# Optimization experiments

Hardware: AMD Instinct MI355X
Metric: run time of the kernel (lower is better)

Reference implementation:

```python
import jax, jax.numpy as jnp
import numpy as np

N, E, F_IN, HID, L_EXTRA, G = 50000, 800000, 128, 128, 3, 256

def gcn_conv(x, W, b, src, dst, norm):
    # PyG GCNConv: out = D^-1/2 (A+I) D^-1/2 (X W) + b  (self-loops included in src/dst)
    xw = x @ W                                  # [N, out]
    msg = xw[src] * norm[:, None]               # [E+N, out]
    return jax.ops.segment_sum(msg, dst, num_segments=N) + b

def setup_inputs() -> dict:
    key = jax.random.key(0)
    ks = jax.random.split(key, 12)
    x = jax.random.normal(ks[0], (N, F_IN), dtype=jnp.float32)
    edge_index = jax.random.randint(ks[1], (2, E), 0, N, dtype=jnp.int64)
    batch = jnp.sort(jax.random.randint(ks[2], (N,), 0, G, dtype=jnp.int64))
    s = 1.0 / np.sqrt(HID)
    W0 = jax.random.uniform(ks[3], (F_IN, HID), jnp.float32, -s, s)
    b0 = jnp.zeros((HID,), jnp.float32)
    Wh = jax.random.uniform(ks[4], (L_EXTRA, HID, HID), jnp.float32, -s, s)
    bh = jnp.zeros((L_EXTRA, HID), jnp.float32)
    s1 = 1.0 / np.sqrt(3 * HID)
    lin1_w = jax.random.uniform(ks[5], (3 * HID, HID), jnp.float32, -s1, s1)
    lin1_b = jax.random.uniform(ks[6], (HID,), jnp.float32, -s1, s1)
    s2 = 1.0 / np.sqrt(HID)
    lin2_w = jax.random.uniform(ks[7], (HID, 2), jnp.float32, -s2, s2)
    lin2_b = jax.random.uniform(ks[8], (2,), jnp.float32, -s2, s2)
    return {"x": x, "edge_index": edge_index, "batch": batch,
            "W0": W0, "b0": b0, "Wh": Wh, "bh": bh,
            "lin1_w": lin1_w, "lin1_b": lin1_b, "lin2_w": lin2_w, "lin2_b": lin2_b}

def reference(x, edge_index, batch, W0, b0, Wh, bh, lin1_w, lin1_b, lin2_w, lin2_b):
    # add self-loops once (shared by all layers)
    loop = jnp.arange(N, dtype=edge_index.dtype)
    src = jnp.concatenate([edge_index[0], loop])
    dst = jnp.concatenate([edge_index[1], loop])
    deg = jax.ops.segment_sum(jnp.ones_like(dst, dtype=x.dtype), dst, num_segments=N)
    dinv = jnp.where(deg > 0, jax.lax.rsqrt(deg), 0.0)
    norm = dinv[src] * dinv[dst]                # [E+N]

    h = jax.nn.relu(gcn_conv(x, W0, b0, src, dst, norm))
    for i in range(L_EXTRA):
        h = jax.nn.relu(gcn_conv(h, Wh[i], bh[i], src, dst, norm))

    # multi-pool over graphs in the batch
    p_sum = jax.ops.segment_sum(h, batch, num_segments=G)
    cnt = jax.ops.segment_sum(jnp.ones((N,), h.dtype), batch, num_segments=G)
    p_mean = p_sum / jnp.maximum(cnt, 1.0)[:, None]
    p_max = jax.ops.segment_max(h, batch, num_segments=G)
    p_max = jnp.where(jnp.isfinite(p_max), p_max, 0.0)  # guard empty graphs
    g = jnp.concatenate([p_sum, p_mean, p_max], axis=1)  # [G, 3*HID]

    g = jax.nn.relu(g @ lin1_w + lin1_b)        # dropout p=0.5 is identity in eval
    logits = g @ lin2_w + lin2_b
    return jax.nn.log_softmax(logits, axis=-1)
```

## Files before the change

kernel.cpp:

```cpp
#include <hip/hip_runtime.h>
#include <hip/hip_fp16.h>
#include <cstddef>

typedef _Float16 f16x8 __attribute__((ext_vector_type(8)));
typedef float f32x4 __attribute__((ext_vector_type(4)));
typedef unsigned short ushort8 __attribute__((ext_vector_type(8)));


__global__ __launch_bounds__(256) void k_zero256(int* __restrict__ a) {
    a[threadIdx.x] = 0;
}

__global__ __launch_bounds__(256) void k_bhist(const int* __restrict__ dst, int* __restrict__ bcnt, int e) {
    __shared__ int lh[256];
    int t = threadIdx.x;
    lh[t] = 0;
    __syncthreads();
    for (int i = blockIdx.x * 256 + t; i < e; i += gridDim.x * 256)
        atomicAdd(&lh[dst[i] >> 8], 1);
    __syncthreads();
    if (lh[t] > 0) atomicAdd(&bcnt[t], lh[t]);
}

__global__ __launch_bounds__(256) void k_bscan(const int* __restrict__ bcnt, int* __restrict__ bebase,
                                               int* __restrict__ bcbase, int* __restrict__ bcur,
                                               int* __restrict__ rowptr, int nbk, int n, int e) {
    __shared__ int se[256], sc[256];
    int t = threadIdx.x;
    int ec = (t < nbk) ? bcnt[t] : 0;
    int nodes = 0;
    if (t < nbk) {
        nodes = n - t * 256;
        if (nodes > 256) nodes = 256;
        if (nodes < 0) nodes = 0;
    }
    se[t] = ec;
    sc[t] = ec + nodes;
    __syncthreads();
    for (int off = 1; off < 256; off <<= 1) {
        int ve = (t >= off) ? se[t - off] : 0;
        int vc = (t >= off) ? sc[t - off] : 0;
        __syncthreads();
        se[t] += ve;
        sc[t] += vc;
        __syncthreads();
    }
    if (t < nbk) {
        bebase[t] = se[t] - ec;
        bcbase[t] = sc[t] - (ec + nodes);
        bcur[t]   = se[t] - ec;
    }
    if (t == 0) {
        bebase[nbk] = e;
        rowptr[n] = e + n;
    }
}

__global__ __launch_bounds__(256) void k_bscatter(const int* __restrict__ src, const int* __restrict__ dst,
                                                  int* __restrict__ bcur, int2* __restrict__ bedges, int e) {
    __shared__ int lh[256];
    __shared__ int gbase[256];
    int t = threadIdx.x;
    lh[t] = 0;
    __syncthreads();
    int base = blockIdx.x * 4096;
    int s_[16], d_[16];
#pragma unroll
    for (int u = 0; u < 16; ++u) {
        int j = base + u * 256 + t;
        if (j < e) {
            s_[u] = src[j];
            d_[u] = dst[j];
            atomicAdd(&lh[d_[u] >> 8], 1);
        } else {
            d_[u] = -1;
        }
    }
    __syncthreads();
    if (lh[t] > 0) gbase[t] = atomicAdd(&bcur[t], lh[t]);
    __syncthreads();
    lh[t] = 0;
    __syncthreads();
#pragma unroll
    for (int u = 0; u < 16; ++u) {
        if (d_[u] >= 0) {
            int bk = d_[u] >> 8;
            int lpos = atomicAdd(&lh[bk], 1);
            bedges[gbase[bk] + lpos] = make_int2(s_[u], d_[u]);
        }
    }
}

__global__ __launch_bounds__(256) void k_bcsr(const int2* __restrict__ bedges, const int* __restrict__ bebase,
                                              const int* __restrict__ bcbase, int* __restrict__ rowptr,
                                              float* __restrict__ dinv, int* __restrict__ csr_s, int n) {
    __shared__ int lh[256], lcur[256];
    int b = blockIdx.x, t = threadIdx.x;
    int n0 = b << 8;
    int nb = n - n0; if (nb > 256) nb = 256;
    int e0 = bebase[b], e1 = bebase[b + 1];
    int cb = bcbase[b];
    lh[t] = 0;
    __syncthreads();
    for (int i = e0 + t; i < e1; i += 256)
        atomicAdd(&lh[bedges[i].y - n0], 1);
    __syncthreads();
    int deg = (t < nb) ? (lh[t] + 1) : 0;
    __syncthreads();
    lh[t] = deg;
    __syncthreads();
    for (int off = 1; off < 256; off <<= 1) {
        int v = (t >= off) ? lh[t - off] : 0;
        __syncthreads();
        lh[t] += v;
        __syncthreads();
    }
    int lrp = lh[t] - deg;
    if (t < nb) {
        rowptr[n0 + t] = cb + lrp;
        dinv[n0 + t] = rsqrtf((float)deg);
    }
    lcur[t] = lrp;
    __syncthreads();
    for (int i = e0 + t; i < e1; i += 256) {
        int2 ed = bedges[i];
        int pos = cb + atomicAdd(&lcur[ed.y - n0], 1);
        csr_s[pos] = ed.x;
    }
    if (t < nb) {
        int pos = cb + atomicAdd(&lcur[t], 1);
        csr_s[pos] = n0 + t;
    }
}

__global__ __launch_bounds__(256) void k_cvt(const float* __restrict__ X, __half* __restrict__ Y, int n8) {
    int i = blockIdx.x * 256 + threadIdx.x;
    if (i >= n8) return;
    float4 v0 = *(const float4*)&X[(size_t)i * 8];
    float4 v1 = *(const float4*)&X[(size_t)i * 8 + 4];
    ushort8 o;
    o[0] = __half_as_ushort(__float2half(v0.x));
    o[1] = __half_as_ushort(__float2half(v0.y));
    o[2] = __half_as_ushort(__float2half(v0.z));
    o[3] = __half_as_ushort(__float2half(v0.w));
    o[4] = __half_as_ushort(__float2half(v1.x));
    o[5] = __half_as_ushort(__float2half(v1.y));
    o[6] = __half_as_ushort(__float2half(v1.z));
    o[7] = __half_as_ushort(__float2half(v1.w));
    *(ushort8*)&Y[(size_t)i * 8] = o;
}

__global__ __launch_bounds__(256) void k_wprep(const float* __restrict__ W0, const float* __restrict__ Wh,
                                               __half* __restrict__ WP) {
    int layer = blockIdx.x;
    const float* W = (layer == 0) ? W0 : Wh + (size_t)(layer - 1) * 16384;
    __half* out = WP + (size_t)layer * 16384;
    int t = threadIdx.x;
    for (int u = 0; u < 64; ++u) {
        int o = u * 256 + t;
        int i  = o & 7;
        int l  = (o >> 3) & 63;
        int kc = (o >> 9) & 3;
        int nt = o >> 11;
        int k   = kc * 32 + ((l >> 4) << 3) + i;
        int col = nt * 16 + (l & 15);
        out[o] = __float2half(W[k * 128 + col]);
    }
}

__global__ __launch_bounds__(256) void k_gemm(const __half* __restrict__ H, const __half* __restrict__ WP,
                                              const float* __restrict__ dinv, __half* __restrict__ O,
                                              int n) {
    __shared__ __half wl[16384];
    const int t = threadIdx.x;
#pragma unroll
    for (int u = 0; u < 8; ++u) {
        int idx = (u * 256 + t) * 8;
        *(ushort8*)&wl[idx] = *(const ushort8*)&WP[idx];
    }
    const int wid = t >> 6, l = t & 63;
    const int row0 = blockIdx.x * 128 + wid * 32;
    const int ar = l & 15, g = l >> 4;

    f16x8 a[2][4];
    float dv[2][4];
#pragma unroll
    for (int mt = 0; mt < 2; ++mt) {
        int row = row0 + mt * 16 + ar;
        int rc = min(row, n - 1);
#pragma unroll
        for (int kc = 0; kc < 4; ++kc)
            a[mt][kc] = *(const f16x8*)&H[(size_t)rc * 128 + kc * 32 + g * 8];
#pragma unroll
        for (int r = 0; r < 4; ++r) {
            int orow = row0 + mt * 16 + g * 4 + r;
            dv[mt][r] = dinv[min(orow, n - 1)];
        }
    }
    __syncthreads();

#pragma unroll
    for (int nt = 0; nt < 8; ++nt) {
        f16x8 b[4];
#pragma unroll
        for (int kc = 0; kc < 4; ++kc)
            b[kc] = *(f16x8*)&wl[((nt * 4 + kc) * 64 + l) * 8];
#pragma unroll
        for (int mt = 0; mt < 2; ++mt) {
            f32x4 acc = {0.f, 0.f, 0.f, 0.f};
#pragma unroll
            for (int kc = 0; kc < 4; ++kc)
                acc = __builtin_amdgcn_mfma_f32_16x16x32_f16(a[mt][kc], b[kc], acc, 0, 0, 0);
#pragma unroll
            for (int r = 0; r < 4; ++r) {
                int orow = row0 + mt * 16 + g * 4 + r;
                if (orow < n)
                    O[(size_t)orow * 128 + nt * 16 + ar] = __float2half(acc[r] * dv[mt][r]);
            }
        }
    }
}

__global__ __launch_bounds__(256) void k_agg(const __half* __restrict__ XW, const int* __restrict__ cs,
                                             const int* __restrict__ rp, const float* __restrict__ dinv,
                                             const float* __restrict__ bias, __half* __restrict__ Hn, int n) {
    int wid  = (blockIdx.x * 256 + threadIdx.x) >> 6;
    int lane = threadIdx.x & 63;
    if (wid >= n) return;
    int s = rp[wid], e = rp[wid + 1];
    const __half2* X2 = (const __half2*)XW;
    float a0 = 0.f, a1 = 0.f, b0v = 0.f, b1v = 0.f, c0v = 0.f, c1v = 0.f, d0v = 0.f, d1v = 0.f;
    for (int base = s; base < e; base += 64) {
        int m = e - base;
        if (m > 64) m = 64;
        int myi = (lane < m) ? cs[base + lane] : 0;
        int j = 0;
        for (; j + 4 <= m; j += 4) {
            int i0 = __shfl(myi, j);
            int i1 = __shfl(myi, j + 1);
            int i2 = __shfl(myi, j + 2);
            int i3 = __shfl(myi, j + 3);
            float2 v0 = __half22float2(X2[(size_t)i0 * 64 + lane]);
            float2 v1 = __half22float2(X2[(size_t)i1 * 64 + lane]);
            float2 v2 = __half22float2(X2[(size_t)i2 * 64 + lane]);
            float2 v3 = __half22float2(X2[(size_t)i3 * 64 + lane]);
            a0 += v0.x; a1 += v0.y;
            b0v += v1.x; b1v += v1.y;
            c0v += v2.x; c1v += v2.y;
            d0v += v3.x; d1v += v3.y;
        }
        for (; j < m; ++j) {
            int i0 = __shfl(myi, j);
            float2 v = __half22float2(X2[(size_t)i0 * 64 + lane]);
            a0 += v.x; a1 += v.y;
        }
    }
    a0 += b0v + c0v + d0v;
    a1 += b1v + c1v + d1v;
    float dvv = dinv[wid];
    int f = lane * 2;
    a0 = fmaxf(fmaf(a0, dvv, bias[f]),     0.f);
    a1 = fmaxf(fmaf(a1, dvv, bias[f + 1]), 0.f);
    ((__half2*)Hn)[(size_t)wid * 64 + lane] = __floats2half2_rn(a0, a1);
}


__global__ __launch_bounds__(256) void k_bounds(const int* __restrict__ batch, int* __restrict__ startg,
                                                int n, int g) {
    int i = blockIdx.x * 256 + threadIdx.x;
    if (i >= n) return;
    int b = batch[i];
    if (i == 0) {
        for (int q = 0; q <= b; ++q) startg[q] = 0;
    } else {
        int pb = batch[i - 1];
        for (int q = pb + 1; q <= b; ++q) startg[q] = i;
    }
    if (i == n - 1) {
        for (int q = b + 1; q <= g; ++q) startg[q] = n;
    }
}

__global__ __launch_bounds__(256) void k_pool(const __half* __restrict__ H, const int* __restrict__ startg,
                                              float* __restrict__ P) {
    __shared__ float ss[256], sm[256];
    int g = blockIdx.x;
    int t = threadIdx.x;
    int f = t & 127, h = t >> 7;
    int s = startg[g], e = startg[g + 1];
    float sum = 0.f, mx = 0.f;
    for (int nidx = s + h; nidx < e; nidx += 2) {
        float v = __half2float(H[(size_t)nidx * 128 + f]);
        sum += v;
        mx = fmaxf(mx, v);
    }
    ss[t] = sum;
    sm[t] = mx;
    __syncthreads();
    if (t < 128) {
        sum = ss[t] + ss[t + 128];
        mx = fmaxf(sm[t], sm[t + 128]);
        float cnt = (float)(e - s);
        P[(size_t)g * 384 + f]       = sum;
        P[(size_t)g * 384 + 128 + f] = sum / fmaxf(cnt, 1.f);
        P[(size_t)g * 384 + 256 + f] = mx;
    }
}

__global__ __launch_bounds__(128) void k_head(const float* __restrict__ P,
                                              const float* __restrict__ w1, const float* __restrict__ b1,
                                              const float* __restrict__ w2, const float* __restrict__ b2,
                                              float* __restrict__ out) {
    __shared__ float gv[384];
    __shared__ float o1[128];
    int g = blockIdx.x, t = threadIdx.x;
    gv[t]       = P[(size_t)g * 384 + t];
    gv[t + 128] = P[(size_t)g * 384 + 128 + t];
    gv[t + 256] = P[(size_t)g * 384 + 256 + t];
    __syncthreads();
    float acc = b1[t];
#pragma unroll 8
    for (int k = 0; k < 384; ++k) acc = fmaf(gv[k], w1[k * 128 + t], acc);
    o1[t] = fmaxf(acc, 0.f);
    __syncthreads();
    if (t < 64) {
        float p0 = o1[t] * w2[t * 2 + 0] + o1[t + 64] * w2[(t + 64) * 2 + 0];
        float p1 = o1[t] * w2[t * 2 + 1] + o1[t + 64] * w2[(t + 64) * 2 + 1];
        for (int off = 32; off > 0; off >>= 1) {
            p0 += __shfl_down(p0, off);
            p1 += __shfl_down(p1, off);
        }
        if (t == 0) {
            float l0 = p0 + b2[0], l1 = p1 + b2[1];
            float m = fmaxf(l0, l1);
            float lse = m + logf(expf(l0 - m) + expf(l1 - m));
            out[g * 2 + 0] = l0 - lse;
            out[g * 2 + 1] = l1 - lse;
        }
    }
}


extern "C" void kernel_launch(void* const* d_in, const int* in_sizes, int n_in,
                              void* d_out, int out_size, void* d_ws, size_t ws_size,
                              hipStream_t stream) {
    const float* x     = (const float*)d_in[0];
    const int*   ei    = (const int*)d_in[1];
    const int*   batch = (const int*)d_in[2];
    const float* W0    = (const float*)d_in[3];
    const float* b0    = (const float*)d_in[4];
    const float* Wh    = (const float*)d_in[5];
    const float* bh    = (const float*)d_in[6];
    const float* l1w   = (const float*)d_in[7];
    const float* l1b   = (const float*)d_in[8];
    const float* l2w   = (const float*)d_in[9];
    const float* l2b   = (const float*)d_in[10];
    float* out = (float*)d_out;

    const int N  = in_sizes[0] / 128;
    const int E  = in_sizes[1] / 2;
    const int G  = out_size / 2;
    const int LX = in_sizes[5] / (128 * 128);
    const int NB = (N + 255) / 256;

    const int* src = ei;
    const int* dst = ei + E;

    char* p = (char*)d_ws;
    auto alloc = [&](size_t bytes) -> void* {
        void* r = (void*)p;
        p += (bytes + 255) & ~(size_t)255;
        return r;
    };
    int*    rowptr = (int*)alloc((size_t)(N + 1) * 4);
    float*  dinv   = (float*)alloc((size_t)N * 4);
    int*    bcnt   = (int*)alloc(1040);
    int*    bebase = (int*)alloc(1040);
    int*    bcbase = (int*)alloc(1040);
    int*    bcur   = (int*)alloc(1040);
    int*    startg = (int*)alloc((size_t)(G + 1) * 4);
    int*    csr_s  = (int*)alloc((size_t)(E + N) * 4);
    int2*   bedges = (int2*)alloc((size_t)E * 8);
    __half* x16    = (__half*)alloc((size_t)N * 128 * 2);
    __half* h16    = (__half*)alloc((size_t)N * 128 * 2);
    __half* xw16   = (__half*)alloc((size_t)N * 128 * 2);
    __half* wp     = (__half*)alloc((size_t)(LX + 1) * 16384 * 2);
    float*  pooled = (float*)alloc((size_t)G * 384 * 4);

    const int nbN = (N + 255) / 256;

    k_wprep<<<LX + 1, 256, 0, stream>>>(W0, Wh, wp);
    k_cvt<<<(N * 16 + 255) / 256, 256, 0, stream>>>(x, x16, N * 16);

    k_zero256<<<1, 256, 0, stream>>>(bcnt);
    k_bhist<<<NB, 256, 0, stream>>>(dst, bcnt, E);
    k_bscan<<<1, 256, 0, stream>>>(bcnt, bebase, bcbase, bcur, rowptr, NB, N, E);
    k_bscatter<<<(E + 4095) / 4096, 256, 0, stream>>>(src, dst, bcur, bedges, E);
    k_bcsr<<<NB, 256, 0, stream>>>(bedges, bebase, bcbase, rowptr, dinv, csr_s, N);

    const int gemmBlocks = (N + 127) / 128;
    const int aggBlocks  = (N + 3) / 4;

    k_gemm<<<gemmBlocks, 256, 0, stream>>>(x16, wp, dinv, xw16, N);
    k_agg<<<aggBlocks, 256, 0, stream>>>(xw16, csr_s, rowptr, dinv, b0, h16, N);
    for (int l = 0; l < LX; ++l) {
        k_gemm<<<gemmBlocks, 256, 0, stream>>>(h16, wp + (size_t)(l + 1) * 16384, dinv, xw16, N);
        k_agg<<<aggBlocks, 256, 0, stream>>>(xw16, csr_s, rowptr, dinv, bh + (size_t)l * 128, h16, N);
    }

    k_bounds<<<nbN, 256, 0, stream>>>(batch, startg, N, G);
    k_pool<<<G, 256, 0, stream>>>(h16, startg, pooled);
    k_head<<<G, 128, 0, stream>>>(pooled, l1w, l1b, l2w, l2b, out);
}
```

Before: 280.7 us.

## Fuse input conversion into first GEMM, merge pooling with head, widen aggregation unroll

```diff
diff --git a/kernel.cpp b/kernel.cpp
--- a/kernel.cpp
+++ b/kernel.cpp
@@ -6,10 +6,6 @@
 typedef float f32x4 __attribute__((ext_vector_type(4)));
 typedef unsigned short ushort8 __attribute__((ext_vector_type(8)));
 
-
-__global__ __launch_bounds__(256) void k_zero256(int* __restrict__ a) {
-    a[threadIdx.x] = 0;
-}
 
 __global__ __launch_bounds__(256) void k_bhist(const int* __restrict__ dst, int* __restrict__ bcnt, int e) {
     __shared__ int lh[256];
@@ -133,29 +129,16 @@
     }
 }
 
-__global__ __launch_bounds__(256) void k_cvt(const float* __restrict__ X, __half* __restrict__ Y, int n8) {
-    int i = blockIdx.x * 256 + threadIdx.x;
-    if (i >= n8) return;
-    float4 v0 = *(const float4*)&X[(size_t)i * 8];
-    float4 v1 = *(const float4*)&X[(size_t)i * 8 + 4];
-    ushort8 o;
-    o[0] = __half_as_ushort(__float2half(v0.x));
-    o[1] = __half_as_ushort(__float2half(v0.y));
-    o[2] = __half_as_ushort(__float2half(v0.z));
-    o[3] = __half_as_ushort(__float2half(v0.w));
-    o[4] = __half_as_ushort(__float2half(v1.x));
-    o[5] = __half_as_ushort(__float2half(v1.y));
-    o[6] = __half_as_ushort(__float2half(v1.z));
-    o[7] = __half_as_ushort(__float2half(v1.w));
-    *(ushort8*)&Y[(size_t)i * 8] = o;
-}
-
 __global__ __launch_bounds__(256) void k_wprep(const float* __restrict__ W0, const float* __restrict__ Wh,
-                                               __half* __restrict__ WP) {
+                                               __half* __restrict__ WP, int* __restrict__ bcnt, int nlayers) {
     int layer = blockIdx.x;
+    int t = threadIdx.x;
+    if (layer >= nlayers) {
+        bcnt[t] = 0;
+        return;
+    }
     const float* W = (layer == 0) ? W0 : Wh + (size_t)(layer - 1) * 16384;
     __half* out = WP + (size_t)layer * 16384;
-    int t = threadIdx.x;
     for (int u = 0; u < 64; ++u) {
         int o = u * 256 + t;
         int i  = o & 7;
@@ -221,6 +204,65 @@
     }
 }
 
+__global__ __launch_bounds__(256) void k_gemm32(const float* __restrict__ H, const __half* __restrict__ WP,
+                                                const float* __restrict__ dinv, __half* __restrict__ O,
+                                                int n) {
+    __shared__ __half wl[16384];
+    const int t = threadIdx.x;
+#pragma unroll
+    for (int u = 0; u < 8; ++u) {
+        int idx = (u * 256 + t) * 8;
+        *(ushort8*)&wl[idx] = *(const ushort8*)&WP[idx];
+    }
+    const int wid = t >> 6, l = t & 63;
+    const int row0 = blockIdx.x * 128 + wid * 32;
+    const int ar = l & 15, g = l >> 4;
+
+    f16x8 a[2][4];
+    float dv[2][4];
+#pragma unroll
+    for (int mt = 0; mt < 2; ++mt) {
+        int row = row0 + mt * 16 + ar;
+        int rc = min(row, n - 1);
+#pragma unroll
+        for (int kc = 0; kc < 4; ++kc) {
+            float4 p0 = *(const float4*)&H[(size_t)rc * 128 + kc * 32 + g * 8];
+            float4 p1 = *(const float4*)&H[(size_t)rc * 128 + kc * 32 + g * 8 + 4];
+            f16x8 av;
+            av[0] = (_Float16)p0.x; av[1] = (_Float16)p0.y; av[2] = (_Float16)p0.z; av[3] = (_Float16)p0.w;
+            av[4] = (_Float16)p1.x; av[5] = (_Float16)p1.y; av[6] = (_Float16)p1.z; av[7] = (_Float16)p1.w;
+            a[mt][kc] = av;
+        }
+#pragma unroll
+        for (int r = 0; r < 4; ++r) {
+            int orow = row0 + mt * 16 + g * 4 + r;
+            dv[mt][r] = dinv[min(orow, n - 1)];
+        }
+    }
+    __syncthreads();
+
+#pragma unroll
+    for (int nt = 0; nt < 8; ++nt) {
+        f16x8 b[4];
+#pragma unroll
+        for (int kc = 0; kc < 4; ++kc)
+            b[kc] = *(f16x8*)&wl[((nt * 4 + kc) * 64 + l) * 8];
+#pragma unroll
+        for (int mt = 0; mt < 2; ++mt) {
+            f32x4 acc = {0.f, 0.f, 0.f, 0.f};
+#pragma unroll
+            for (int kc = 0; kc < 4; ++kc)
+                acc = __builtin_amdgcn_mfma_f32_16x16x32_f16(a[mt][kc], b[kc], acc, 0, 0, 0);
+#pragma unroll
+            for (int r = 0; r < 4; ++r) {
+                int orow = row0 + mt * 16 + g * 4 + r;
+                if (orow < n)
+                    O[(size_t)orow * 128 + nt * 16 + ar] = __float2half(acc[r] * dv[mt][r]);
+            }
+        }
+    }
+}
+
 __global__ __launch_bounds__(256) void k_agg(const __half* __restrict__ XW, const int* __restrict__ cs,
                                              const int* __restrict__ rp, const float* __restrict__ dinv,
                                              const float* __restrict__ bias, __half* __restrict__ Hn, int n) {
@@ -229,34 +271,33 @@
     if (wid >= n) return;
     int s = rp[wid], e = rp[wid + 1];
     const __half2* X2 = (const __half2*)XW;
-    float a0 = 0.f, a1 = 0.f, b0v = 0.f, b1v = 0.f, c0v = 0.f, c1v = 0.f, d0v = 0.f, d1v = 0.f;
+    float ax[8], ay[8];
+#pragma unroll
+    for (int u = 0; u < 8; ++u) { ax[u] = 0.f; ay[u] = 0.f; }
     for (int base = s; base < e; base += 64) {
         int m = e - base;
         if (m > 64) m = 64;
         int myi = (lane < m) ? cs[base + lane] : 0;
         int j = 0;
-        for (; j + 4 <= m; j += 4) {
-            int i0 = __shfl(myi, j);
-            int i1 = __shfl(myi, j + 1);
-            int i2 = __shfl(myi, j + 2);
-            int i3 = __shfl(myi, j + 3);
-            float2 v0 = __half22float2(X2[(size_t)i0 * 64 + lane]);
-            float2 v1 = __half22float2(X2[(size_t)i1 * 64 + lane]);
-            float2 v2 = __half22float2(X2[(size_t)i2 * 64 + lane]);
-            float2 v3 = __half22float2(X2[(size_t)i3 * 64 + lane]);
-            a0 += v0.x; a1 += v0.y;
-            b0v += v1.x; b1v += v1.y;
-            c0v += v2.x; c1v += v2.y;
-            d0v += v3.x; d1v += v3.y;
+        for (; j + 8 <= m; j += 8) {
+            int idx[8];
+#pragma unroll
+            for (int u = 0; u < 8; ++u) idx[u] = __shfl(myi, j + u);
+            float2 v[8];
+#pragma unroll
+            for (int u = 0; u < 8; ++u) v[u] = __half22float2(X2[(size_t)idx[u] * 64 + lane]);
+#pragma unroll
+            for (int u = 0; u < 8; ++u) { ax[u] += v[u].x; ay[u] += v[u].y; }
         }
         for (; j < m; ++j) {
             int i0 = __shfl(myi, j);
             float2 v = __half22float2(X2[(size_t)i0 * 64 + lane]);
-            a0 += v.x; a1 += v.y;
-        }
-    }
-    a0 += b0v + c0v + d0v;
-    a1 += b1v + c1v + d1v;
+            ax[j & 7] += v.x;
+            ay[j & 7] += v.y;
+        }
+    }
+    float a0 = (ax[0] + ax[1]) + (ax[2] + ax[3]) + ((ax[4] + ax[5]) + (ax[6] + ax[7]));
+    float a1 = (ay[0] + ay[1]) + (ay[2] + ay[3]) + ((ay[4] + ay[5]) + (ay[6] + ay[7]));
     float dvv = dinv[wid];
     int f = lane * 2;
     a0 = fmaxf(fmaf(a0, dvv, bias[f]),     0.f);
@@ -264,30 +305,27 @@
     ((__half2*)Hn)[(size_t)wid * 64 + lane] = __floats2half2_rn(a0, a1);
 }
 
-
-__global__ __launch_bounds__(256) void k_bounds(const int* __restrict__ batch, int* __restrict__ startg,
-                                                int n, int g) {
-    int i = blockIdx.x * 256 + threadIdx.x;
-    if (i >= n) return;
-    int b = batch[i];
-    if (i == 0) {
-        for (int q = 0; q <= b; ++q) startg[q] = 0;
-    } else {
-        int pb = batch[i - 1];
-        for (int q = pb + 1; q <= b; ++q) startg[q] = i;
-    }
-    if (i == n - 1) {
-        for (int q = b + 1; q <= g; ++q) startg[q] = n;
-    }
-}
-
-__global__ __launch_bounds__(256) void k_pool(const __half* __restrict__ H, const int* __restrict__ startg,
-                                              float* __restrict__ P) {
+__global__ __launch_bounds__(256) void k_poolhead(const __half* __restrict__ H, const int* __restrict__ batch,
+                                                  const float* __restrict__ w1, const float* __restrict__ b1,
+                                                  const float* __restrict__ w2, const float* __restrict__ b2,
+                                                  float* __restrict__ out, int n) {
     __shared__ float ss[256], sm[256];
-    int g = blockIdx.x;
-    int t = threadIdx.x;
+    __shared__ float gv[384];
+    __shared__ float o1[128];
+    __shared__ int bnd[2];
+    int g = blockIdx.x, t = threadIdx.x;
+    if (t < 2) {
+        int key = g + t;
+        int lo = 0, hi = n;
+        while (lo < hi) {
+            int mid = (lo + hi) >> 1;
+            if (batch[mid] < key) lo = mid + 1; else hi = mid;
+        }
+        bnd[t] = lo;
+    }
+    __syncthreads();
+    int s = bnd[0], e = bnd[1];
     int f = t & 127, h = t >> 7;
-    int s = startg[g], e = startg[g + 1];
     float sum = 0.f, mx = 0.f;
     for (int nidx = s + h; nidx < e; nidx += 2) {
         float v = __half2float(H[(size_t)nidx * 128 + f]);
@@ -301,27 +339,17 @@
         sum = ss[t] + ss[t + 128];
         mx = fmaxf(sm[t], sm[t + 128]);
         float cnt = (float)(e - s);
-        P[(size_t)g * 384 + f]       = sum;
-        P[(size_t)g * 384 + 128 + f] = sum / fmaxf(cnt, 1.f);
-        P[(size_t)g * 384 + 256 + f] = mx;
-    }
-}
-
-__global__ __launch_bounds__(128) void k_head(const float* __restrict__ P,
-                                              const float* __restrict__ w1, const float* __restrict__ b1,
-                                              const float* __restrict__ w2, const float* __restrict__ b2,
-                                              float* __restrict__ out) {
-    __shared__ float gv[384];
-    __shared__ float o1[128];
-    int g = blockIdx.x, t = threadIdx.x;
-    gv[t]       = P[(size_t)g * 384 + t];
-    gv[t + 128] = P[(size_t)g * 384 + 128 + t];
-    gv[t + 256] = P[(size_t)g * 384 + 256 + t];
-    __syncthreads();
-    float acc = b1[t];
+        gv[t]       = sum;
+        gv[128 + t] = sum / fmaxf(cnt, 1.f);
+        gv[256 + t] = mx;
+    }
+    __syncthreads();
+    if (t < 128) {
+        float acc = b1[t];
 #pragma unroll 8
-    for (int k = 0; k < 384; ++k) acc = fmaf(gv[k], w1[k * 128 + t], acc);
-    o1[t] = fmaxf(acc, 0.f);
+        for (int k = 0; k < 384; ++k) acc = fmaf(gv[k], w1[k * 128 + t], acc);
+        o1[t] = fmaxf(acc, 0.f);
+    }
     __syncthreads();
     if (t < 64) {
         float p0 = o1[t] * w2[t * 2 + 0] + o1[t + 64] * w2[(t + 64) * 2 + 0];
@@ -378,21 +406,14 @@
     int*    bebase = (int*)alloc(1040);
     int*    bcbase = (int*)alloc(1040);
     int*    bcur   = (int*)alloc(1040);
-    int*    startg = (int*)alloc((size_t)(G + 1) * 4);
     int*    csr_s  = (int*)alloc((size_t)(E + N) * 4);
     int2*   bedges = (int2*)alloc((size_t)E * 8);
-    __half* x16    = (__half*)alloc((size_t)N * 128 * 2);
     __half* h16    = (__half*)alloc((size_t)N * 128 * 2);
     __half* xw16   = (__half*)alloc((size_t)N * 128 * 2);
     __half* wp     = (__half*)alloc((size_t)(LX + 1) * 16384 * 2);
-    float*  pooled = (float*)alloc((size_t)G * 384 * 4);
-
-    const int nbN = (N + 255) / 256;
-
-    k_wprep<<<LX + 1, 256, 0, stream>>>(W0, Wh, wp);
-    k_cvt<<<(N * 16 + 255) / 256, 256, 0, stream>>>(x, x16, N * 16);
-
-    k_zero256<<<1, 256, 0, stream>>>(bcnt);
+
+    k_wprep<<<LX + 2, 256, 0, stream>>>(W0, Wh, wp, bcnt, LX + 1);
+
     k_bhist<<<NB, 256, 0, stream>>>(dst, bcnt, E);
     k_bscan<<<1, 256, 0, stream>>>(bcnt, bebase, bcbase, bcur, rowptr, NB, N, E);
     k_bscatter<<<(E + 4095) / 4096, 256, 0, stream>>>(src, dst, bcur, bedges, E);
@@ -401,14 +422,12 @@
     const int gemmBlocks = (N + 127) / 128;
     const int aggBlocks  = (N + 3) / 4;
 
-    k_gemm<<<gemmBlocks, 256, 0, stream>>>(x16, wp, dinv, xw16, N);
+    k_gemm32<<<gemmBlocks, 256, 0, stream>>>(x, wp, dinv, xw16, N);
     k_agg<<<aggBlocks, 256, 0, stream>>>(xw16, csr_s, rowptr, dinv, b0, h16, N);
     for (int l = 0; l < LX; ++l) {
         k_gemm<<<gemmBlocks, 256, 0, stream>>>(h16, wp + (size_t)(l + 1) * 16384, dinv, xw16, N);
         k_agg<<<aggBlocks, 256, 0, stream>>>(xw16, csr_s, rowptr, dinv, bh + (size_t)l * 128, h16, N);
     }
 
-    k_bounds<<<nbN, 256, 0, stream>>>(batch, startg, N, G);
-    k_pool<<<G, 256, 0, stream>>>(h16, startg, pooled);
-    k_head<<<G, 128, 0, stream>>>(pooled, l1w, l1b, l2w, l2b, out);
-}
+    k_poolhead<<<G, 256, 0, stream>>>(h16, batch, l1w, l1b, l2w, l2b, out, N);
+}
```

Measured after the change: 279.4 us. No clear change (-0.5%).
